# Kernel tuning notes

Measured on AMD Instinct MI355X. Metric: run time of the kernel, lower is better.

Reference implementation:

```python
import jax, jax.numpy as jnp
import numpy as np

EMBED_DIM = 1024
NUM_HEADS = 16
SEQ_LEN = 2048
BATCH = 2
LN_EPS = 1e-5


def setup_inputs() -> dict:
    key = jax.random.key(0)
    ks = jax.random.split(key, 12)
    d = EMBED_DIM
    s = 1.0 / np.sqrt(d)
    inp = {
        "x": jax.random.normal(ks[0], (BATCH, SEQ_LEN, d), dtype=jnp.float32),
        "ln1_g": jnp.ones((d,), jnp.float32),
        "ln1_b": jnp.zeros((d,), jnp.float32),
        "ln2_g": jnp.ones((d,), jnp.float32),
        "ln2_b": jnp.zeros((d,), jnp.float32),
        "W_qkv": jax.random.normal(ks[1], (d, 3 * d), jnp.float32) * s,
        "b_qkv": jnp.zeros((3 * d,), jnp.float32),
        "W_proj": jax.random.normal(ks[2], (d, d), jnp.float32) * s,
        "b_proj": jnp.zeros((d,), jnp.float32),
        "W_fc": jax.random.normal(ks[3], (d, 4 * d), jnp.float32) * s,
        "b_fc": jnp.zeros((4 * d,), jnp.float32),
        "W_out": jax.random.normal(ks[4], (4 * d, d), jnpp_dummy := jnp.float32) * (1.0 / np.sqrt(4 * d)),
        "b_out": jnp.zeros((d,), jnp.float32),
    }
    return inp


def _layernorm(x, g, b):
    mu = jnp.mean(x, axis=-1, keepdims=True)
    var = jnp.mean(jnp.square(x - mu), axis=-1, keepdims=True)
    return (x - mu) * jax.lax.rsqrt(var + LN_EPS) * g + b


def _block(x, ln1_g, ln1_b, ln2_g, ln2_b, W_qkv, b_qkv, W_proj, b_proj, W_fc, b_fc, W_out, b_out):
    B, S, D = x.shape
    H = NUM_HEADS
    hd = D // H
    h = _layernorm(x, ln1_g, ln1_b)
    qkv = h @ W_qkv + b_qkv  # [B,S,3D]
    q, k, v = jnp.split(qkv, 3, axis=-1)
    # [B,H,S,hd]
    q = q.reshape(B, S, H, hd).transpose(0, 2, 1, 3)
    k = k.reshape(B, S, H, hd).transpose(0, 2, 1, 3)
    v = v.reshape(B, S, H, hd).transpose(0, 2, 1, 3)
    attn = jnp.einsum("bhqd,bhkd->bhqk", q, k) / np.sqrt(hd).astype(np.float32)
    causal = jnp.tril(jnp.ones((S, S), dtype=bool))
    attn = jnp.where(causal, attn, -jnp.inf)
    attn = jax.nn.softmax(attn, axis=-1)
    y = jnp.einsum("bhqk,bhkd->bhqd", attn, v)
    y = y.transpose(0, 2, 1, 3).reshape(B, S, D)
    y = y @ W_proj + b_proj
    x = x + y
    h2 = _layernorm(x, ln2_g, ln2_b)
    m = jax.nn.relu(h2 @ W_fc + b_fc) @ W_out + b_out
    return x + m


def reference(x, ln1_g, ln1_b, ln2_g, ln2_b, W_qkv, b_qkv, W_proj, b_proj, W_fc, b_fc, W_out, b_out):
    return _block(x, ln1_g, ln1_b, ln2_g, ln2_b, W_qkv, b_qkv, W_proj, b_proj, W_fc, b_fc, W_out, b_out)
```

## Files before the change

### kernel.cpp

```cpp
#include <hip/hip_runtime.h>

typedef unsigned short u16;
typedef __attribute__((ext_vector_type(8))) __bf16 bf16x8;
typedef __attribute__((ext_vector_type(4))) float f32x4;

#define DEV __device__ __forceinline__

DEV u16 f2bf(float f) {
  unsigned u = __float_as_uint(f);
  u += 0x7fffu + ((u >> 16) & 1u);
  return (u16)(u >> 16);
}
DEV float bf2f(u16 u) { return __uint_as_float((unsigned)u << 16); }

DEV void gl_lds16(const void* g, void* l) {
  __builtin_amdgcn_global_load_lds(
      (const __attribute__((address_space(1))) void*)(uintptr_t)g,
      (__attribute__((address_space(3))) void*)(unsigned)(uintptr_t)l, 16, 0, 0);
}

DEV float wave_sum64(float v) {
#pragma unroll
  for (int off = 32; off > 0; off >>= 1) v += __shfl_down(v, off);
  return v;
}

DEV void ln_body(const float4 v, const float* g, const float* be, u16* out_row, int t,
                 float* red) {
  const int w = t >> 6, L = t & 63;
  float s = v.x + v.y + v.z + v.w;
  s = wave_sum64(s);
  if (L == 0) red[w] = s;
  __syncthreads();
  const float mean = (red[0] + red[1] + red[2] + red[3]) * (1.0f / 1024.0f);
  const float dx = v.x - mean, dy = v.y - mean, dz = v.z - mean, dw = v.w - mean;
  float q = dx * dx + dy * dy + dz * dz + dw * dw;
  q = wave_sum64(q);
  if (L == 0) red[4 + w] = q;
  __syncthreads();
  const float var = (red[4] + red[5] + red[6] + red[7]) * (1.0f / 1024.0f);
  const float rs = rsqrtf(var + 1e-5f);
  const float4 gg = reinterpret_cast<const float4*>(g)[t];
  const float4 bb = reinterpret_cast<const float4*>(be)[t];
  ushort4 o;
  o.x = f2bf(dx * rs * gg.x + bb.x);
  o.y = f2bf(dy * rs * gg.y + bb.y);
  o.z = f2bf(dz * rs * gg.z + bb.z);
  o.w = f2bf(dw * rs * gg.w + bb.w);
  reinterpret_cast<ushort4*>(out_row)[t] = o;
}

__global__ __launch_bounds__(256) void prep_kernel(
    const float* __restrict__ x, const float* __restrict__ ln1g,
    const float* __restrict__ ln1b, u16* __restrict__ hbuf,
    const float* __restrict__ Wqkv, u16* __restrict__ wt_qkv,
    const float* __restrict__ Wproj, u16* __restrict__ wt_proj,
    const float* __restrict__ Wfc, u16* __restrict__ wt_fc,
    const float* __restrict__ Wout, u16* __restrict__ wt_out) {
  __shared__ float smem[32 * 33];
  int id = blockIdx.x;
  const int t = threadIdx.x;
  if (id < 4096) {
    const float4 v = reinterpret_cast<const float4*>(x + (size_t)id * 1024)[t];
    ln_body(v, ln1g, ln1b, hbuf + (size_t)id * 1024, t, smem);
    return;
  }
  id -= 4096;
  const float* W;
  u16* Wt;
  int K, N, nbx;
  if (id < 3072) {
    W = Wqkv; Wt = wt_qkv; K = 1024; N = 3072; nbx = 96;
  } else if (id < 3072 + 1024) {
    id -= 3072; W = Wproj; Wt = wt_proj; K = 1024; N = 1024; nbx = 32;
  } else if (id < 3072 + 1024 + 4096) {
    id -= 3072 + 1024; W = Wfc; Wt = wt_fc; K = 1024; N = 4096; nbx = 128;
  } else {
    id -= 3072 + 1024 + 4096; W = Wout; Wt = wt_out; K = 4096; N = 1024; nbx = 32;
  }
  float(*tile)[33] = (float(*)[33])smem;
  const int c0 = (id % nbx) * 32, r0 = (id / nbx) * 32;
  const int tx = t & 31, ty = t >> 5;
#pragma unroll
  for (int j = 0; j < 4; ++j)
    tile[ty + j * 8][tx] = W[(size_t)(r0 + ty + j * 8) * N + c0 + tx];
  __syncthreads();
#pragma unroll
  for (int j = 0; j < 4; ++j) {
    const int n = c0 + ty + j * 8, k = r0 + tx;
    Wt[(size_t)n * K + k] = f2bf(tile[tx][ty + j * 8]);
  }
}

__global__ __launch_bounds__(256) void proj_reduce_ln(const float* __restrict__ x,
                                                      const float* __restrict__ bias,
                                                      const u16* __restrict__ P0,
                                                      const u16* __restrict__ P1,
                                                      const float* __restrict__ g,
                                                      const float* __restrict__ be,
                                                      float* __restrict__ x2,
                                                      u16* __restrict__ hbuf) {
  const int row = blockIdx.x, t = threadIdx.x;
  const size_t off = (size_t)row * 1024;
  __shared__ float red[8];
  const float4 xv = reinterpret_cast<const float4*>(x + off)[t];
  const float4 bv = reinterpret_cast<const float4*>(bias)[t];
  const ushort4 p0 = reinterpret_cast<const ushort4*>(P0 + off)[t];
  const ushort4 p1 = reinterpret_cast<const ushort4*>(P1 + off)[t];
  float4 v;
  v.x = xv.x + bv.x + bf2f(p0.x) + bf2f(p1.x);
  v.y = xv.y + bv.y + bf2f(p0.y) + bf2f(p1.y);
  v.z = xv.z + bv.z + bf2f(p0.z) + bf2f(p1.z);
  v.w = xv.w + bv.w + bf2f(p0.w) + bf2f(p1.w);
  reinterpret_cast<float4*>(x2 + off)[t] = v;
  ln_body(v, g, be, hbuf + off, t, red);
}

__global__ __launch_bounds__(256) void out_reduce(const float* __restrict__ x2,
                                                  const float* __restrict__ bias,
                                                  const u16* __restrict__ P0,
                                                  const u16* __restrict__ P1,
                                                  float* __restrict__ dout) {
  const int row = blockIdx.x, t = threadIdx.x;
  const size_t off = (size_t)row * 1024;
  const float4 xv = reinterpret_cast<const float4*>(x2 + off)[t];
  const float4 bv = reinterpret_cast<const float4*>(bias)[t];
  const ushort4 a = reinterpret_cast<const ushort4*>(P0 + off)[t];
  const ushort4 b = reinterpret_cast<const ushort4*>(P1 + off)[t];
  float4 o;
  o.x = xv.x + bv.x + bf2f(a.x) + bf2f(b.x);
  o.y = xv.y + bv.y + bf2f(a.y) + bf2f(b.y);
  o.z = xv.z + bv.z + bf2f(a.z) + bf2f(b.z);
  o.w = xv.w + bv.w + bf2f(a.w) + bf2f(b.w);
  reinterpret_cast<float4*>(dout + off)[t] = o;
}

enum { F_BIAS = 1, F_RESID = 2, F_RELU = 4, F_BF16 = 8, F_PART4 = 32, F_VT = 64 };

template <int FLAGS>
__global__ __launch_bounds__(256, 2) void gemm_bt(const u16* __restrict__ A,
                                                  const u16* __restrict__ Bt,
                                                  const float* __restrict__ bias,
                                                  const float* __restrict__ resid,
                                                  void* __restrict__ Cout,
                                                  u16* __restrict__ pp0, u16* __restrict__ pp1,
                                                  u16* __restrict__ pp2, u16* __restrict__ pp3,
                                                  int M, int N, int K, int Kst) {
  __shared__ __attribute__((aligned(16))) u16 sA[2][128 * 32];
  __shared__ __attribute__((aligned(16))) u16 sB[2][128 * 32];

  const int gx = gridDim.x, gy = gridDim.y;
  const int tilesPerZ = gx * gy;
  int lin = (blockIdx.z * gy + blockIdx.y) * gx + blockIdx.x;
  const int total = tilesPerZ * gridDim.z;
  if (!(total & 7)) lin = (lin & 7) * (total >> 3) + (lin >> 3);
  const int zz = lin / tilesPerZ;
  const int pid = lin - zz * tilesPerZ;
  const int npg = gx << 3;
  const int gid = pid / npg;
  const int rem = pid - gid * npg;
  const int fm = gid << 3;
  const int gsm = (gy - fm < 8) ? (gy - fm) : 8;
  const int bm = fm + rem % gsm;
  const int bn = rem / gsm;

  const int t = threadIdx.x, w = t >> 6, L = t & 63, quad = L >> 4, l15 = L & 15;
  const int wm = w >> 1, wn = w & 1;
  const int m0 = bm * 128, n0 = bn * 128;
  const u16* Ag = A + (size_t)m0 * Kst + (size_t)zz * K;
  const u16* Bg = Bt + (size_t)n0 * Kst + (size_t)zz * K;

  f32x4 acc[4][4] = {};

  for (int k0 = 0; k0 < K; k0 += 64) {
    __syncthreads();
#pragma unroll
    for (int h = 0; h < 2; ++h) {
#pragma unroll
      for (int i = 0; i < 2; ++i) {
        const int cp = i * 256 + t, rr = cp >> 2, cc = (cp & 3) << 3;
        gl_lds16(Ag + (size_t)rr * Kst + k0 + h * 32 + cc, &sA[h][(i * 256 + w * 64) * 8]);
      }
#pragma unroll
      for (int i = 0; i < 2; ++i) {
        const int cp = i * 256 + t, rr = cp >> 2, cc = (cp & 3) << 3;
        gl_lds16(Bg + (size_t)rr * Kst + k0 + h * 32 + cc, &sB[h][(i * 256 + w * 64) * 8]);
      }
    }
    __syncthreads();

#pragma unroll
    for (int h = 0; h < 2; ++h) {
      bf16x8 af[4], bfr[4];
#pragma unroll
      for (int m = 0; m < 4; ++m)
        af[m] = *(const bf16x8*)&sA[h][(wm * 64 + m * 16 + l15) * 32 + quad * 8];
#pragma unroll
      for (int n = 0; n < 4; ++n)
        bfr[n] = *(const bf16x8*)&sB[h][(wn * 64 + n * 16 + l15) * 32 + quad * 8];
#pragma unroll
      for (int m = 0; m < 4; ++m)
#pragma unroll
        for (int n = 0; n < 4; ++n)
          acc[m][n] =
              __builtin_amdgcn_mfma_f32_16x16x32_bf16(af[m], bfr[n], acc[m][n], 0, 0, 0);
    }
  }

  if ((FLAGS & F_VT) && n0 >= 2048) {
#pragma unroll
    for (int m = 0; m < 4; ++m) {
#pragma unroll
      for (int n = 0; n < 4; ++n) {
        const int col = n0 + wn * 64 + n * 16 + l15;
        const float bv = bias[col];
        const int hh = (col - 2048) >> 6, dd = col & 63;
        const int srow = m0 + wm * 64 + m * 16 + quad * 4;
        const int bb = srow >> 11, ss = srow & 2047;
        ushort4 tmp;
        tmp.x = f2bf(acc[m][n][0] + bv);
        tmp.y = f2bf(acc[m][n][1] + bv);
        tmp.z = f2bf(acc[m][n][2] + bv);
        tmp.w = f2bf(acc[m][n][3] + bv);
        *(ushort4*)(pp0 + ((size_t)((bb * 16 + hh) * 64 + dd)) * 2048 + ss) = tmp;
      }
    }
    return;
  }

  u16* pbase = nullptr;
  if (FLAGS & F_PART4)
    pbase = (zz == 0) ? pp0 : (zz == 1) ? pp1 : (zz == 2) ? pp2 : pp3;

#pragma unroll
  for (int m = 0; m < 4; ++m) {
#pragma unroll
    for (int n = 0; n < 4; ++n) {
      const int col = n0 + wn * 64 + n * 16 + l15;
      const float bv = (FLAGS & F_BIAS) ? bias[col] : 0.0f;
#pragma unroll
      for (int rr = 0; rr < 4; ++rr) {
        const int row = m0 + wm * 64 + m * 16 + quad * 4 + rr;
        if (FLAGS & F_PART4) {
          pbase[(size_t)row * N + col] = f2bf(acc[m][n][rr]);
        } else {
          float v = acc[m][n][rr] + bv;
          if (FLAGS & F_RESID) v += resid[(size_t)row * N + col];
          if (FLAGS & F_RELU) v = fmaxf(v, 0.0f);
          if (FLAGS & F_BF16)
            ((u16*)Cout)[(size_t)row * N + col] = f2bf(v);
          else
            ((float*)Cout)[(size_t)row * N + col] = v;
        }
      }
    }
  }
}

__global__ __launch_bounds__(512) void flash_attn(const u16* __restrict__ qkv,
                                                  const u16* __restrict__ Vt,
                                                  u16* __restrict__ y,
                                                  float* __restrict__ acc0,
                                                  float* __restrict__ acc1,
                                                  float* __restrict__ lacc0,
                                                  float* __restrict__ lacc1) {
  constexpr int S = 2048, D3 = 3072, D = 1024;
  constexpr float Csc = 0.125f * 1.44269504088896f;
  __shared__ __attribute__((aligned(16))) u16 sK[2][64 * 64];
  __shared__ __attribute__((aligned(16))) u16 sV[2][64 * 64];
  __shared__ __attribute__((aligned(16))) u16 sP[8][2 * 16 * 40];

  const int bid = blockIdx.x;
  const int bh = bid & 31;
  const int e = bid >> 5;
  int qt, it0, it1, part;
  if (e < 8) {
    qt = 8 + e; it0 = 0; it1 = 16; part = 1;
  } else {
    const int j = (e - 8) >> 1;
    if (((e - 8) & 1) == 0) {
      qt = 7 - j; it0 = 0; it1 = 2 * qt + 2; part = 0;
    } else {
      qt = 15 - j; it0 = 16; it1 = 2 * qt + 2; part = 2;
    }
  }
  const int b = bh >> 4, h = bh & 15;
  const int q0 = qt * 128;

  const int t = threadIdx.x, w = t >> 6, L = t & 63, quad = L >> 4, l15 = L & 15;
  const int qw = q0 + w * 16;

  const u16* qbase = qkv + (size_t)(b * S) * D3 + h * 64;
  const u16* Kbase = qbase + D;
  const u16* Vbase = Vt + (size_t)((b * 16 + h) * 64) * S;

  const int srow = t >> 3;
  const int k8 = ((t & 7) ^ (srow & 7)) << 3;
  const u16* Ksrc = Kbase + (size_t)srow * D3 + k8;
  const u16* Vsrc = Vbase + (size_t)srow * S + k8;

  bf16x8 aQ[2];
#pragma unroll
  for (int kk = 0; kk < 2; ++kk)
    aQ[kk] = *(const bf16x8*)(qbase + (size_t)(qw + l15) * D3 + kk * 32 + quad * 8);

  bf16x8 ones;
#pragma unroll
  for (int i = 0; i < 8; ++i) ones[i] = (__bf16)1.0f;

  f32x4 acc[4] = {};
  f32x4 lacc = {};

  u16* sPw = sP[w];
  const int swz = l15 & 7;

  gl_lds16(Ksrc + (size_t)(it0 * 64) * D3, &sK[0][(w * 64) * 8]);
  gl_lds16(Vsrc + it0 * 64, &sV[0][(w * 64) * 8]);

  int cur = 0;
  for (int it = it0; it < it1; ++it) {
    const int kv0 = it * 64;
    if (it + 1 < it1) {
      const int kvn = kv0 + 64;
      gl_lds16(Ksrc + (size_t)kvn * D3, &sK[cur ^ 1][(w * 64) * 8]);
      gl_lds16(Vsrc + kvn, &sV[cur ^ 1][(w * 64) * 8]);
      asm volatile("s_waitcnt vmcnt(2)" ::: "memory");
    } else {
      asm volatile("s_waitcnt vmcnt(0)" ::: "memory");
    }
    __builtin_amdgcn_s_barrier();

    const u16* sKc = sK[cur];
    const u16* sVc = sV[cur];

    f32x4 s[4] = {};
    __builtin_amdgcn_s_setprio(1);
#pragma unroll
    for (int kk = 0; kk < 2; ++kk) {
#pragma unroll
      for (int n = 0; n < 4; ++n) {
        const bf16x8 bK =
            *(const bf16x8*)&sKc[(n * 16 + l15) * 64 + ((kk * 4 + quad) ^ swz) * 8];
        s[n] = __builtin_amdgcn_mfma_f32_16x16x32_bf16(aQ[kk], bK, s[n], 0, 0, 0);
      }
    }
    __builtin_amdgcn_s_setprio(0);

    if (kv0 + 63 > qw) {
#pragma unroll
      for (int n = 0; n < 4; ++n) {
        const int col = kv0 + n * 16 + l15;
#pragma unroll
        for (int r = 0; r < 4; ++r) {
          const int row = qw + quad * 4 + r;
          const float p = __builtin_amdgcn_exp2f(s[n][r] * Csc);
          s[n][r] = (col > row) ? 0.0f : p;
        }
      }
    } else {
#pragma unroll
      for (int n = 0; n < 4; ++n)
#pragma unroll
        for (int r = 0; r < 4; ++r) s[n][r] = __builtin_amdgcn_exp2f(s[n][r] * Csc);
    }

#pragma unroll
    for (int n = 0; n < 4; ++n)
#pragma unroll
      for (int r = 0; r < 4; ++r)
        sPw[(n >> 1) * 640 + (quad * 4 + r) * 40 + (n & 1) * 16 + l15] = f2bf(s[n][r]);

    __builtin_amdgcn_s_setprio(1);
#pragma unroll
    for (int kk = 0; kk < 2; ++kk) {
      const bf16x8 aP = *(const bf16x8*)&sPw[kk * 640 + l15 * 40 + quad * 8];
      lacc = __builtin_amdgcn_mfma_f32_16x16x32_bf16(aP, ones, lacc, 0, 0, 0);
#pragma unroll
      for (int dn = 0; dn < 4; ++dn) {
        const bf16x8 bV =
            *(const bf16x8*)&sVc[(dn * 16 + l15) * 64 + ((kk * 4 + quad) ^ swz) * 8];
        acc[dn] = __builtin_amdgcn_mfma_f32_16x16x32_bf16(aP, bV, acc[dn], 0, 0, 0);
      }
    }
    __builtin_amdgcn_s_setprio(0);

    asm volatile("s_waitcnt lgkmcnt(0)" ::: "memory");
    __builtin_amdgcn_s_barrier();
    cur ^= 1;
  }

  if (part == 0) {
#pragma unroll
    for (int r = 0; r < 4; ++r) {
      const float inv = 1.0f / lacc[r];
      const int row = qw + quad * 4 + r;
      u16* yb = y + (size_t)(b * S + row) * D + h * 64 + l15;
#pragma unroll
      for (int dn = 0; dn < 4; ++dn) yb[dn * 16] = f2bf(acc[dn][r] * inv);
    }
  } else {
    float* accP = (part == 1) ? acc0 : acc1;
    float* laccP = (part == 1) ? lacc0 : lacc1;
#pragma unroll
    for (int r = 0; r < 4; ++r) {
      const int row = qw + quad * 4 + r;
      const int g = (bh << 10) + (row - 1024);
      float* ap = accP + (size_t)g * 64 + l15;
#pragma unroll
      for (int dn = 0; dn < 4; ++dn) ap[dn * 16] = acc[dn][r];
      if (l15 == 0) laccP[g] = lacc[r];
    }
  }
}

__global__ __launch_bounds__(256) void attn_combine(const float* __restrict__ acc0,
                                                    const float* __restrict__ acc1,
                                                    const float* __restrict__ lacc0,
                                                    const float* __restrict__ lacc1,
                                                    u16* __restrict__ y) {
  const int t = threadIdx.x;
  const int g = blockIdx.x * 4 + (t >> 6);
  const int d = t & 63;
  const int bh = g >> 10, ri = g & 1023;
  const int b = bh >> 4, h = bh & 15;
  const int row = 1024 + ri;
  const size_t po = (size_t)g * 64 + d;
  const float l = lacc0[g] + lacc1[g];
  const float v = (acc0[po] + acc1[po]) / l;
  y[((size_t)(b * 2048 + row)) * 1024 + h * 64 + d] = f2bf(v);
}

extern "C" void kernel_launch(void* const* d_in, const int* in_sizes, int n_in,
                              void* d_out, int out_size, void* d_ws, size_t ws_size,
                              hipStream_t stream) {
  const float* x = (const float*)d_in[0];
  const float* ln1g = (const float*)d_in[1];
  const float* ln1b = (const float*)d_in[2];
  const float* ln2g = (const float*)d_in[3];
  const float* ln2b = (const float*)d_in[4];
  const float* Wqkv = (const float*)d_in[5];
  const float* bqkv = (const float*)d_in[6];
  const float* Wproj = (const float*)d_in[7];
  const float* bproj = (const float*)d_in[8];
  const float* Wfc = (const float*)d_in[9];
  const float* bfc = (const float*)d_in[10];
  const float* Wout = (const float*)d_in[11];
  const float* bout = (const float*)d_in[12];

  char* ws = (char*)d_ws;
  const size_t MB = 1u << 20;
  u16* wt_out = (u16*)(ws + 0 * MB);
  u16* hbuf = (u16*)(ws + 8 * MB);
  float* x2 = (float*)(ws + 16 * MB);
  u16* ybuf = (u16*)(ws + 32 * MB);
  u16* qkvb = (u16*)(ws + 40 * MB);
  u16* vtb = (u16*)(ws + 64 * MB);
  u16* wt_qkv = (u16*)(ws + 72 * MB);
  u16* wt_proj = (u16*)(ws + 78 * MB);
  u16* wt_fc = (u16*)(ws + 80 * MB);
  u16* projP0 = (u16*)(ws + 40 * MB);
  u16* projP1 = (u16*)(ws + 48 * MB);
  u16* m1 = (u16*)(ws + 40 * MB);
  u16* po0 = (u16*)(ws + 8 * MB);
  u16* po1 = (u16*)(ws + 32 * MB);
  float* facc0 = (float*)(ws + 8 * MB);
  float* facc1 = (float*)(ws + 16 * MB);
  float* flacc0 = (float*)(ws + 24 * MB);
  float* flacc1 = (float*)(ws + 25 * MB);

  prep_kernel<<<4096 + 3072 + 1024 + 4096 + 4096, 256, 0, stream>>>(
      x, ln1g, ln1b, hbuf, Wqkv, wt_qkv, Wproj, wt_proj, Wfc, wt_fc, Wout, wt_out);

  gemm_bt<F_BIAS | F_BF16 | F_VT><<<dim3(24, 32), 256, 0, stream>>>(
      hbuf, wt_qkv, bqkv, nullptr, qkvb, vtb, nullptr, nullptr, nullptr,
      4096, 3072, 1024, 1024);
  flash_attn<<<768, 512, 0, stream>>>(qkvb, vtb, ybuf, facc0, facc1, flacc0, flacc1);
  attn_combine<<<8192, 256, 0, stream>>>(facc0, facc1, flacc0, flacc1, ybuf);

  gemm_bt<F_PART4><<<dim3(8, 32, 2), 256, 0, stream>>>(
      ybuf, wt_proj, nullptr, nullptr, nullptr, projP0, projP1, nullptr, nullptr,
      4096, 1024, 512, 1024);
  proj_reduce_ln<<<4096, 256, 0, stream>>>(x, bproj, projP0, projP1, ln2g, ln2b, x2, hbuf);

  gemm_bt<F_BIAS | F_RELU | F_BF16><<<dim3(32, 32), 256, 0, stream>>>(
      hbuf, wt_fc, bfc, nullptr, m1, nullptr, nullptr, nullptr, nullptr,
      4096, 4096, 1024, 1024);

  gemm_bt<F_PART4><<<dim3(8, 32, 2), 256, 0, stream>>>(
      m1, wt_out, nullptr, nullptr, nullptr, po0, po1, nullptr, nullptr,
      4096, 1024, 2048, 4096);
  out_reduce<<<4096, 256, 0, stream>>>(x2, bout, po0, po1, (float*)d_out);
}
```

Baseline: 313.7 us.

## Replace split-K partial buffers and out_reduce with atomic adds into output

The residual-plus-bias initialisation of the output moves into proj_reduce_ln, and the final split-K GEMM now atomically adds its fp32 accumulators straight into the output instead of writing two bf16 partial buffers. This drops the out_reduce kernel launch and the partial-buffer write/read traffic. In exchange it issues scalar fp32 atomics that touch each output element twice, adds an extra output write in proj_reduce_ln, and makes the summation order nondeterministic.

```diff
diff --git a/kernel.cpp b/kernel.cpp
--- a/kernel.cpp
+++ b/kernel.cpp
@@ -98,7 +98,9 @@
                                                       const u16* __restrict__ P1,
                                                       const float* __restrict__ g,
                                                       const float* __restrict__ be,
+                                                      const float* __restrict__ bout,
                                                       float* __restrict__ x2,
+                                                      float* __restrict__ dout,
                                                       u16* __restrict__ hbuf) {
   const int row = blockIdx.x, t = threadIdx.x;
   const size_t off = (size_t)row * 1024;
@@ -113,29 +115,18 @@
   v.z = xv.z + bv.z + bf2f(p0.z) + bf2f(p1.z);
   v.w = xv.w + bv.w + bf2f(p0.w) + bf2f(p1.w);
   reinterpret_cast<float4*>(x2 + off)[t] = v;
+  const float4 ov = reinterpret_cast<const float4*>(bout)[t];
+  float4 d;
+  d.x = v.x + ov.x;
+  d.y = v.y + ov.y;
+  d.z = v.z + ov.z;
+  d.w = v.w + ov.w;
+  reinterpret_cast<float4*>(dout + off)[t] = d;
   ln_body(v, g, be, hbuf + off, t, red);
 }
 
-__global__ __launch_bounds__(256) void out_reduce(const float* __restrict__ x2,
-                                                  const float* __restrict__ bias,
-                                                  const u16* __restrict__ P0,
-                                                  const u16* __restrict__ P1,
-                                                  float* __restrict__ dout) {
-  const int row = blockIdx.x, t = threadIdx.x;
-  const size_t off = (size_t)row * 1024;
-  const float4 xv = reinterpret_cast<const float4*>(x2 + off)[t];
-  const float4 bv = reinterpret_cast<const float4*>(bias)[t];
-  const ushort4 a = reinterpret_cast<const ushort4*>(P0 + off)[t];
-  const ushort4 b = reinterpret_cast<const ushort4*>(P1 + off)[t];
-  float4 o;
-  o.x = xv.x + bv.x + bf2f(a.x) + bf2f(b.x);
-  o.y = xv.y + bv.y + bf2f(a.y) + bf2f(b.y);
-  o.z = xv.z + bv.z + bf2f(a.z) + bf2f(b.z);
-  o.w = xv.w + bv.w + bf2f(a.w) + bf2f(b.w);
-  reinterpret_cast<float4*>(dout + off)[t] = o;
-}
-
-enum { F_BIAS = 1, F_RESID = 2, F_RELU = 4, F_BF16 = 8, F_PART4 = 32, F_VT = 64 };
+enum { F_BIAS = 1, F_RESID = 2, F_RELU = 4, F_BF16 = 8, F_PART4 = 32, F_VT = 64,
+       F_ATOMIC = 128 };
 
 template <int FLAGS>
 __global__ __launch_bounds__(256, 2) void gemm_bt(const u16* __restrict__ A,
@@ -223,6 +214,22 @@
         tmp.z = f2bf(acc[m][n][2] + bv);
         tmp.w = f2bf(acc[m][n][3] + bv);
         *(ushort4*)(pp0 + ((size_t)((bb * 16 + hh) * 64 + dd)) * 2048 + ss) = tmp;
+      }
+    }
+    return;
+  }
+
+  if (FLAGS & F_ATOMIC) {
+#pragma unroll
+    for (int m = 0; m < 4; ++m) {
+#pragma unroll
+      for (int n = 0; n < 4; ++n) {
+        const int col = n0 + wn * 64 + n * 16 + l15;
+#pragma unroll
+        for (int rr = 0; rr < 4; ++rr) {
+          const int row = m0 + wm * 64 + m * 16 + quad * 4 + rr;
+          atomicAdd((float*)Cout + (size_t)row * N + col, acc[m][n][rr]);
+        }
       }
     }
     return;
@@ -461,8 +468,6 @@
   u16* projP0 = (u16*)(ws + 40 * MB);
   u16* projP1 = (u16*)(ws + 48 * MB);
   u16* m1 = (u16*)(ws + 40 * MB);
-  u16* po0 = (u16*)(ws + 8 * MB);
-  u16* po1 = (u16*)(ws + 32 * MB);
   float* facc0 = (float*)(ws + 8 * MB);
   float* facc1 = (float*)(ws + 16 * MB);
   float* flacc0 = (float*)(ws + 24 * MB);
@@ -480,14 +485,14 @@
   gemm_bt<F_PART4><<<dim3(8, 32, 2), 256, 0, stream>>>(
       ybuf, wt_proj, nullptr, nullptr, nullptr, projP0, projP1, nullptr, nullptr,
       4096, 1024, 512, 1024);
-  proj_reduce_ln<<<4096, 256, 0, stream>>>(x, bproj, projP0, projP1, ln2g, ln2b, x2, hbuf);
+  proj_reduce_ln<<<4096, 256, 0, stream>>>(x, bproj, projP0, projP1, ln2g, ln2b,
+                                           bout, x2, (float*)d_out, hbuf);
 
   gemm_bt<F_BIAS | F_RELU | F_BF16><<<dim3(32, 32), 256, 0, stream>>>(
       hbuf, wt_fc, bfc, nullptr, m1, nullptr, nullptr, nullptr, nullptr,
       4096, 4096, 1024, 1024);
 
-  gemm_bt<F_PART4><<<dim3(8, 32, 2), 256, 0, stream>>>(
-      m1, wt_out, nullptr, nullptr, nullptr, po0, po1, nullptr, nullptr,
+  gemm_bt<F_ATOMIC><<<dim3(8, 32, 2), 256, 0, stream>>>(
+      m1, wt_out, nullptr, nullptr, d_out, nullptr, nullptr, nullptr, nullptr,
       4096, 1024, 2048, 4096);
-  out_reduce<<<4096, 256, 0, stream>>>(x2, bout, po0, po1, (float*)d_out);
-}
+}
```

After: 330.9 us. 1.05x slower.
